# Optimization experiments

Measured on AMD Instinct MI355X. Metric: run time of the kernel, lower is better.

Reference implementation:

```python
import jax, jax.numpy as jnp
import numpy as np

V_DIM = 2048
Q_DIM = 1024
B = 64
K = 36


def setup_inputs() -> dict:
    key = jax.random.key(0)
    ks = jax.random.split(key, 6)
    s1 = 1.0 / np.sqrt(2 * V_DIM + Q_DIM)
    s2 = 1.0 / np.sqrt(V_DIM)
    s3 = 1.0 / np.sqrt(Q_DIM)
    return {
        "v": jax.random.normal(ks[0], (B, K, V_DIM), dtype=jnp.float32),
        "q": jax.random.normal(ks[1], (B, Q_DIM), dtype=jnp.float32),
        "W1": jax.random.normal(ks[2], (V_DIM, 2 * V_DIM + Q_DIM), dtype=jnp.float32) * s1,
        "b1": jnp.zeros((V_DIM,), dtype=jnp.float32),
        "W2": jax.random.normal(ks[3], (V_DIM, V_DIM), dtype=jnp.float32) * s2,
        "b2": jnp.zeros((V_DIM,), dtype=jnp.float32),
        "W3": jax.random.normal(ks[4], (Q_DIM, Q_DIM), dtype=jnp.float32) * s3,
        "b3": jnp.zeros((Q_DIM,), dtype=jnp.float32),
    }


def reference(v, q, W1, b1, W2, b2, W3, b3):
    # FCNet = (weight-normed) Linear + ReLU; dropout disabled (eval / p=0).
    vd = W2.shape[0]
    # q embedding: [B, q_dim]
    q_emb = jax.nn.relu(q @ W3.T + b3)
    # Decompose linear1(concat(v_i, v_j, q_emb)) into three matmuls.
    Wa = W1[:, :vd]            # acts on v_i
    Wb = W1[:, vd:2 * vd]      # acts on v_j
    Wc = W1[:, 2 * vd:]        # acts on q_emb
    a = jnp.einsum('bkd,vd->bkv', v, Wa)          # [B, K, v_dim]
    bpart = jnp.einsum('bkd,vd->bkv', v, Wb)      # [B, K, v_dim]
    c = jnp.einsum('bq,vq->bv', q_emb, Wc) + b1   # [B, v_dim]
    # Pairwise ReLU then sum over j: [B, K_i, K_j, v_dim] -> [B, K, v_dim]
    pair = jax.nn.relu(a[:, :, None, :] + bpart[:, None, :, :] + c[:, None, None, :])
    x = jnp.sum(pair, axis=2)
    # linear2 + ReLU
    return jax.nn.relu(jnp.einsum('bkv,wv->bkw', x, W2) + b2)
```

## Files before the change

### kernel.cpp

```cpp
#include <hip/hip_runtime.h>

#define V_DIMC 2048
#define Q_DIMC 1024
#define BATCH  64
#define KC     36
#define MROWS  (BATCH * KC)
#define W1LD   (2 * V_DIMC + Q_DIMC)

typedef __bf16 bf16_t;
typedef __attribute__((ext_vector_type(8))) __bf16 bf16x8;
typedef __attribute__((ext_vector_type(4))) __bf16 bf16x4;
typedef __attribute__((ext_vector_type(4))) float f32x4;

__device__ __forceinline__ void gload16(const bf16_t* g, bf16_t* l) {
    __builtin_amdgcn_global_load_lds(
        (const __attribute__((address_space(1))) unsigned int*)(g),
        (__attribute__((address_space(3))) unsigned int*)(l), 16, 0, 0);
}

#define MFMAI(a, b, c) __builtin_amdgcn_mfma_f32_16x16x32_bf16(a, b, c, 0, 0, 0)
#define BARX() __builtin_amdgcn_s_barrier()
#define LGKM0() asm volatile("s_waitcnt lgkmcnt(0)" ::: "memory")
#define VMC(n)  asm volatile("s_waitcnt vmcnt(" #n ")" ::: "memory")

__global__ __launch_bounds__(256) void conv_all(const float* __restrict__ v,
                                                const float* __restrict__ q,
                                                const float* __restrict__ W1,
                                                const float* __restrict__ W2,
                                                const float* __restrict__ W3,
                                                bf16_t* __restrict__ Wab,
                                                bf16_t* __restrict__ W2b,
                                                bf16_t* __restrict__ vb,
                                                bf16_t* __restrict__ W3b,
                                                bf16_t* __restrict__ Wcb,
                                                bf16_t* __restrict__ qb) {
    const int t = blockIdx.x * 256 + threadIdx.x;
    const float* src;
    bf16_t* dst;
    if (t < 2097152) {
        size_t idx = (size_t)t * 4;
        int row = (int)(idx >> 11), col = (int)(idx & 2047);
        src = (row < 2048) ? W1 + (size_t)row * W1LD + col
                           : W1 + (size_t)(row - 2048) * W1LD + V_DIMC + col;
        dst = Wab + idx;
    } else if (t < 3145728) {
        size_t idx = (size_t)(t - 2097152) * 4;
        src = W2 + idx; dst = W2b + idx;
    } else if (t < 4325376) {
        size_t idx = (size_t)(t - 3145728) * 4;
        src = v + idx; dst = vb + idx;
    } else if (t < 4587520) {
        size_t idx = (size_t)(t - 4325376) * 4;
        src = W3 + idx; dst = W3b + idx;
    } else if (t < 5111808) {
        size_t idx = (size_t)(t - 4587520) * 4;
        int row = (int)(idx >> 10), col = (int)(idx & 1023);
        src = W1 + (size_t)row * W1LD + 2 * V_DIMC + col;
        dst = Wcb + idx;
    } else {
        size_t idx = (size_t)(t - 5111808) * 4;
        src = q + idx; dst = qb + idx;
    }
    float4 f = *reinterpret_cast<const float4*>(src);
    bf16x4 o;
    o[0] = (bf16_t)f.x; o[1] = (bf16_t)f.y; o[2] = (bf16_t)f.z; o[3] = (bf16_t)f.w;
    *reinterpret_cast<bf16x4*>(dst) = o;
}

template <int NDIM, int KDIM, int MODE>
__global__ __launch_bounds__(256) void mfma_gemm64(const bf16_t* __restrict__ A,
                                                   const bf16_t* __restrict__ B,
                                                   void* __restrict__ out,
                                                   const float* __restrict__ bias) {
    __shared__ bf16_t As[64][32];
    __shared__ bf16_t Bs[128][32];
    const int n0 = blockIdx.x * 128;
    const int tid = threadIdx.x;
    const int w = tid >> 6, l = tid & 63;
    const int srow = tid >> 2;
    const int scol = (tid & 3) * 8;
    const bf16_t* Ag  = A + (size_t)srow * KDIM + scol;
    const bf16_t* Bg0 = B + (size_t)(n0 + srow) * KDIM + scol;
    const bf16_t* Bg1 = B + (size_t)(n0 + 64 + srow) * KDIM + scol;
    bf16_t* ldsA  = &As[w * 16][0];
    bf16_t* ldsB0 = &Bs[w * 16][0];
    bf16_t* ldsB1 = &Bs[64 + w * 16][0];
    const int fr = l & 15, fko = (l >> 4) * 8;

    f32x4 acc[4][2] = {};
    for (int k0 = 0; k0 < KDIM; k0 += 32) {
        gload16(Ag + k0, ldsA);
        gload16(Bg0 + k0, ldsB0);
        gload16(Bg1 + k0, ldsB1);
        __syncthreads();
        bf16x8 af[4], bfr[2];
#pragma unroll
        for (int m = 0; m < 4; ++m)
            af[m] = *reinterpret_cast<const bf16x8*>(&As[m * 16 + fr][fko]);
#pragma unroll
        for (int n = 0; n < 2; ++n)
            bfr[n] = *reinterpret_cast<const bf16x8*>(&Bs[w * 32 + n * 16 + fr][fko]);
#pragma unroll
        for (int m = 0; m < 4; ++m)
#pragma unroll
            for (int n = 0; n < 2; ++n)
                acc[m][n] = MFMAI(af[m], bfr[n], acc[m][n]);
        __syncthreads();
    }
    const int col = l & 15, rb = (l >> 4) * 4;
#pragma unroll
    for (int m = 0; m < 4; ++m)
#pragma unroll
        for (int n = 0; n < 2; ++n) {
            const int gn = n0 + w * 32 + n * 16 + col;
            const float bs = bias[gn];
#pragma unroll
            for (int r = 0; r < 4; ++r) {
                const int gm = m * 16 + rb + r;
                const float val = acc[m][n][r];
                if (MODE == 0)
                    ((bf16_t*)out)[(size_t)gm * NDIM + gn] = (bf16_t)fmaxf(val + bs, 0.f);
                else
                    ((float*)out)[(size_t)gm * NDIM + gn] = val + bs;
            }
        }
}

template <int MODE>
__global__ __launch_bounds__(512) void gemm8p(const bf16_t* __restrict__ A,
                                              const bf16_t* __restrict__ Bm,
                                              bf16_t* __restrict__ out0,
                                              bf16_t* __restrict__ out1,
                                              bf16_t* __restrict__ out2) {
    constexpr int K = 2048;
    const int z = (MODE == 2) ? (int)blockIdx.z : 0;
    const int NT = (MODE == 2) ? ((z == 2) ? 10 : 11) : 32;
    const int kb = (MODE == 2) ? z * 704 : 0;
    __shared__ bf16_t lds[2][4][8192];
    const int tid = threadIdx.x;
    const int w = tid >> 6, l = tid & 63;
    const int wm = w >> 2, wn = w & 3;
    const int m0 = blockIdx.y * 256;
    const int n0 = blockIdx.x * 256;
    const size_t sK = (size_t)K;

    const int arow = tid >> 3;
    const bf16_t* gA = A + (size_t)(m0 + arow) * sK + kb
                         + (size_t)(((tid & 7) ^ (arow & 7)) << 3);
    const int brow = tid >> 2;
    const bf16_t* gB = Bm + (size_t)(n0 + brow) * sK + kb
                          + (size_t)(((tid & 3) ^ ((tid >> 3) & 3)) << 3);
    const int stW = w * 512;

#define STGA(h, T) do {                                                        \
        const bf16_t* g_ = gA + (size_t)((h) * 128) * sK + (size_t)(T) * 64;   \
        bf16_t* d_ = &lds[(T) & 1][h][stW];                                    \
        gload16(g_, d_);                                                       \
        gload16(g_ + (size_t)64 * sK, d_ + 4096);                              \
    } while (0)
#define STGB(ks, T) do {                                                       \
        const bf16_t* g_ = gB + (size_t)(T) * 64 + (ks) * 32;                  \
        bf16_t* d_ = &lds[(T) & 1][2 + (ks)][stW];                             \
        gload16(g_, d_);                                                       \
        gload16(g_ + (size_t)128 * sK, d_ + 4096);                             \
    } while (0)

    const int fr = l & 15, lq = l >> 4;
    const int sw0 = (lq ^ (fr & 7)) << 4;
    const int sw1 = ((4 | lq) ^ (fr & 7)) << 4;
    const int bsw = (lq ^ ((fr >> 1) & 3)) << 4;
    const int aro = fr * 128;
    const int bro = (wn * 64 + fr) * 64 + bsw;

    f32x4 acc[8][4] = {};

    STGA(0, 0); STGA(1, 0); STGB(0, 0); STGB(1, 0);
    STGB(0, 1); STGB(1, 1);
    VMC(4);
    BARX();

    for (int T = 0; T < NT; ++T) {
        const char* pa  = (const char*)&lds[T & 1][wm][0];
        const char* pb0 = (const char*)&lds[T & 1][2][0];
        const char* pb1 = (const char*)&lds[T & 1][3][0];
        bf16x8 aF[4], bF[4];

#pragma unroll
        for (int mi = 0; mi < 4; ++mi)
            aF[mi] = *(const bf16x8*)(pa + mi * 2048 + aro + sw0);
#pragma unroll
        for (int ni = 0; ni < 4; ++ni)
            bF[ni] = *(const bf16x8*)(pb0 + bro + ni * 1024);
        if (T + 1 < NT) { STGA(0, T + 1); STGA(1, T + 1); }
        BARX(); LGKM0();
        __builtin_amdgcn_s_setprio(1);
#pragma unroll
        for (int mi = 0; mi < 4; ++mi)
#pragma unroll
            for (int ni = 0; ni < 4; ++ni)
                acc[mi][ni] = MFMAI(aF[mi], bF[ni], acc[mi][ni]);
        __builtin_amdgcn_s_setprio(0);
        BARX();

#pragma unroll
        for (int mi = 0; mi < 4; ++mi)
            aF[mi] = *(const bf16x8*)(pa + 8192 + mi * 2048 + aro + sw0);
        BARX(); LGKM0();
        __builtin_amdgcn_s_setprio(1);
#pragma unroll
        for (int mi = 0; mi < 4; ++mi)
#pragma unroll
            for (int ni = 0; ni < 4; ++ni)
                acc[4 + mi][ni] = MFMAI(aF[mi], bF[ni], acc[4 + mi][ni]);
        __builtin_amdgcn_s_setprio(0);
        BARX();

#pragma unroll
        for (int mi = 0; mi < 4; ++mi)
            aF[mi] = *(const bf16x8*)(pa + mi * 2048 + aro + sw1);
#pragma unroll
        for (int ni = 0; ni < 4; ++ni)
            bF[ni] = *(const bf16x8*)(pb1 + bro + ni * 1024);
        if (T + 2 < NT) STGB(0, T + 2);
        BARX(); LGKM0();
        __builtin_amdgcn_s_setprio(1);
#pragma unroll
        for (int mi = 0; mi < 4; ++mi)
#pragma unroll
            for (int ni = 0; ni < 4; ++ni)
                acc[mi][ni] = MFMAI(aF[mi], bF[ni], acc[mi][ni]);
        __builtin_amdgcn_s_setprio(0);
        BARX();

#pragma unroll
        for (int mi = 0; mi < 4; ++mi)
            aF[mi] = *(const bf16x8*)(pa + 8192 + mi * 2048 + aro + sw1);
        if (T + 2 < NT) STGB(1, T + 2);
        BARX(); LGKM0();
        __builtin_amdgcn_s_setprio(1);
#pragma unroll
        for (int mi = 0; mi < 4; ++mi)
#pragma unroll
            for (int ni = 0; ni < 4; ++ni)
                acc[4 + mi][ni] = MFMAI(aF[mi], bF[ni], acc[4 + mi][ni]);
        __builtin_amdgcn_s_setprio(0);
        if (T < NT - 2) { VMC(4); } else { VMC(0); }
        BARX();
    }
#undef STGA
#undef STGB

    bf16_t* o;
    int gn0;
    if (MODE == 0) {
        if (n0 < V_DIMC) { o = out0; gn0 = n0; }
        else             { o = out1; gn0 = n0 - V_DIMC; }
    } else {
        o = (z == 0) ? out0 : (z == 1) ? out1 : out2;
        gn0 = n0;
    }
    const int rb = lq * 4;
#pragma unroll
    for (int mi = 0; mi < 8; ++mi)
#pragma unroll
        for (int ni = 0; ni < 4; ++ni) {
            const size_t gm = (size_t)(m0 + wm * 128 + mi * 16 + rb);
            const int gn = gn0 + wn * 64 + ni * 16 + fr;
#pragma unroll
            for (int r = 0; r < 4; ++r)
                o[(gm + r) * V_DIMC + gn] = (bf16_t)acc[mi][ni][r];
        }
}

__global__ __launch_bounds__(256) void reduce_out(const bf16_t* __restrict__ p0,
                                                  const bf16_t* __restrict__ p1,
                                                  const bf16_t* __restrict__ p2,
                                                  const float* __restrict__ b2,
                                                  float* __restrict__ out) {
    const size_t t = (size_t)blockIdx.x * 256 + threadIdx.x;
    const size_t idx = t * 8;
    bf16x8 a = *reinterpret_cast<const bf16x8*>(p0 + idx);
    bf16x8 b = *reinterpret_cast<const bf16x8*>(p1 + idx);
    bf16x8 c = *reinterpret_cast<const bf16x8*>(p2 + idx);
    const int col = (int)(idx & (V_DIMC - 1));
    float4 r0, r1;
    float* rr[2] = {&r0.x, &r1.x};
#pragma unroll
    for (int h = 0; h < 2; ++h)
#pragma unroll
        for (int j = 0; j < 4; ++j)
            rr[h][j] = fmaxf((float)a[h * 4 + j] + (float)b[h * 4 + j] +
                             (float)c[h * 4 + j] + b2[col + h * 4 + j], 0.f);
    *reinterpret_cast<float4*>(out + idx) = r0;
    *reinterpret_cast<float4*>(out + idx + 4) = r1;
}

__global__ __launch_bounds__(256) void pair_kernel(const bf16_t* __restrict__ A,
                                                   const bf16_t* __restrict__ Bp,
                                                   const float* __restrict__ cbuf,
                                                   bf16_t* __restrict__ X) {
    const int v = blockIdx.x * 256 + threadIdx.x;
    const int b = blockIdx.y;
    const float cc = cbuf[b * V_DIMC + v];
    const bf16_t* Ab = A + (size_t)b * KC * V_DIMC + v;
    const bf16_t* Bb = Bp + (size_t)b * KC * V_DIMC + v;
    float av[KC], bv[KC];
#pragma unroll
    for (int k = 0; k < KC; ++k) {
        av[k] = (float)Ab[(size_t)k * V_DIMC] + cc;
        bv[k] = (float)Bb[(size_t)k * V_DIMC];
    }
    bf16_t* Xb = X + (size_t)b * KC * V_DIMC + v;
#pragma unroll
    for (int k = 0; k < KC; ++k) {
        float s = 0.f;
#pragma unroll
        for (int j = 0; j < KC; ++j) s += fmaxf(av[k] + bv[j], 0.f);
        Xb[(size_t)k * V_DIMC] = (bf16_t)s;
    }
}

extern "C" void kernel_launch(void* const* d_in, const int* in_sizes, int n_in,
                              void* d_out, int out_size, void* d_ws, size_t ws_size,
                              hipStream_t stream) {
    const float* v  = (const float*)d_in[0];
    const float* q  = (const float*)d_in[1];
    const float* W1 = (const float*)d_in[2];
    const float* b1 = (const float*)d_in[3];
    const float* W2 = (const float*)d_in[4];
    const float* b2 = (const float*)d_in[5];
    const float* W3 = (const float*)d_in[6];
    const float* b3 = (const float*)d_in[7];
    float* out = (float*)d_out;

    char* wsb = (char*)d_ws;
    bf16_t* Wab_b = (bf16_t*)wsb;
    bf16_t* W2b   = (bf16_t*)(wsb + 16777216ull);
    bf16_t* vb    = (bf16_t*)(wsb + 25165824ull);
    bf16_t* Abf   = (bf16_t*)(wsb + 34603008ull);
    bf16_t* W3b   = (bf16_t*)(wsb + 34603008ull);
    bf16_t* Wcb   = (bf16_t*)(wsb + 34603008ull + 2097152);
    bf16_t* qb    = (bf16_t*)(wsb + 34603008ull + 6291456);
    bf16_t* Bbf   = (bf16_t*)(wsb + 44040192ull);
    bf16_t* qemb  = (bf16_t*)(wsb + 53477376ull);
    float*  cbuf  = (float*) (wsb + 53608448ull);
    bf16_t* Xb    = Wab_b;

    conv_all<<<dim3(20032), 256, 0, stream>>>(v, q, W1, W2, W3, Wab_b, W2b, vb, W3b, Wcb, qb);
    mfma_gemm64<Q_DIMC, Q_DIMC, 0><<<dim3(Q_DIMC / 128), 256, 0, stream>>>(qb, W3b, qemb, b3);
    mfma_gemm64<V_DIMC, Q_DIMC, 1><<<dim3(V_DIMC / 128), 256, 0, stream>>>(qemb, Wcb, cbuf, b1);

    gemm8p<0><<<dim3(4096 / 256, MROWS / 256), 512, 0, stream>>>(vb, Wab_b, Abf, Bbf, nullptr);
    pair_kernel<<<dim3(V_DIMC / 256, BATCH), 256, 0, stream>>>(Abf, Bbf, cbuf, Xb);
    gemm8p<2><<<dim3(V_DIMC / 256, MROWS / 256, 3), 512, 0, stream>>>(Xb, W2b, Abf, Bbf, vb);
    reduce_out<<<dim3((MROWS * V_DIMC / 8) / 256), 256, 0, stream>>>(Abf, Bbf, vb, b2, out);
}
```

Measured before the change: 156.9 us.

## Split-K the small q GEMMs across warps and shrink first big GEMM M-tile

Replaces the small 64-row q-embedding and c GEMMs with a kernel that splits K across 8 warps, loads fragments straight from global memory, and reduces the partial sums through LDS. Each block now covers 64 output columns, giving twice as many blocks for these latency-bound GEMMs. The large v GEMM is templated on M-fragment count and uses 192-row tiles, so the grid is 12 row tiles instead of 9 and spreads better across the CUs. The trade-offs are extra LDS reduction traffic in the q GEMMs and smaller A tiles, which lower MFMA reuse per B load.

```diff
diff --git a/kernel.cpp b/kernel.cpp
--- a/kernel.cpp
+++ b/kernel.cpp
@@ -67,80 +67,94 @@
     *reinterpret_cast<bf16x4*>(dst) = o;
 }
 
-template <int NDIM, int KDIM, int MODE>
-__global__ __launch_bounds__(256) void mfma_gemm64(const bf16_t* __restrict__ A,
-                                                   const bf16_t* __restrict__ B,
-                                                   void* __restrict__ out,
-                                                   const float* __restrict__ bias) {
-    __shared__ bf16_t As[64][32];
-    __shared__ bf16_t Bs[128][32];
-    const int n0 = blockIdx.x * 128;
+template <int MODE>
+__global__ __launch_bounds__(512) void qgemm(const bf16_t* __restrict__ A,
+                                             const bf16_t* __restrict__ B,
+                                             void* __restrict__ out,
+                                             const float* __restrict__ bias) {
+    constexpr int K = 1024;
+    constexpr int NDIM = (MODE == 0) ? Q_DIMC : V_DIMC;
+    __shared__ float red[8][4096];
     const int tid = threadIdx.x;
     const int w = tid >> 6, l = tid & 63;
-    const int srow = tid >> 2;
-    const int scol = (tid & 3) * 8;
-    const bf16_t* Ag  = A + (size_t)srow * KDIM + scol;
-    const bf16_t* Bg0 = B + (size_t)(n0 + srow) * KDIM + scol;
-    const bf16_t* Bg1 = B + (size_t)(n0 + 64 + srow) * KDIM + scol;
-    bf16_t* ldsA  = &As[w * 16][0];
-    bf16_t* ldsB0 = &Bs[w * 16][0];
-    bf16_t* ldsB1 = &Bs[64 + w * 16][0];
-    const int fr = l & 15, fko = (l >> 4) * 8;
-
-    f32x4 acc[4][2] = {};
-    for (int k0 = 0; k0 < KDIM; k0 += 32) {
-        gload16(Ag + k0, ldsA);
-        gload16(Bg0 + k0, ldsB0);
-        gload16(Bg1 + k0, ldsB1);
-        __syncthreads();
-        bf16x8 af[4], bfr[2];
-#pragma unroll
-        for (int m = 0; m < 4; ++m)
-            af[m] = *reinterpret_cast<const bf16x8*>(&As[m * 16 + fr][fko]);
-#pragma unroll
-        for (int n = 0; n < 2; ++n)
-            bfr[n] = *reinterpret_cast<const bf16x8*>(&Bs[w * 32 + n * 16 + fr][fko]);
-#pragma unroll
-        for (int m = 0; m < 4; ++m)
-#pragma unroll
-            for (int n = 0; n < 2; ++n)
-                acc[m][n] = MFMAI(af[m], bfr[n], acc[m][n]);
-        __syncthreads();
-    }
-    const int col = l & 15, rb = (l >> 4) * 4;
-#pragma unroll
-    for (int m = 0; m < 4; ++m)
-#pragma unroll
-        for (int n = 0; n < 2; ++n) {
-            const int gn = n0 + w * 32 + n * 16 + col;
-            const float bs = bias[gn];
-#pragma unroll
-            for (int r = 0; r < 4; ++r) {
-                const int gm = m * 16 + rb + r;
-                const float val = acc[m][n][r];
-                if (MODE == 0)
-                    ((bf16_t*)out)[(size_t)gm * NDIM + gn] = (bf16_t)fmaxf(val + bs, 0.f);
-                else
-                    ((float*)out)[(size_t)gm * NDIM + gn] = val + bs;
-            }
-        }
-}
-
-template <int MODE>
+    const int n0 = blockIdx.x * 64;
+    const int fr = l & 15, lq = l >> 4;
+    const bf16_t* Ab = A + (size_t)(w * 128) + lq * 8;
+    const bf16_t* Bb = B + (size_t)n0 * K + (size_t)(w * 128) + lq * 8;
+
+    f32x4 acc[4][4] = {};
+#pragma unroll
+    for (int ks = 0; ks < 4; ++ks) {
+        bf16x8 aF[4], bF[4];
+#pragma unroll
+        for (int mi = 0; mi < 4; ++mi)
+            aF[mi] = *(const bf16x8*)(Ab + (size_t)(mi * 16 + fr) * K + ks * 32);
+#pragma unroll
+        for (int ni = 0; ni < 4; ++ni)
+            bF[ni] = *(const bf16x8*)(Bb + (size_t)(ni * 16 + fr) * K + ks * 32);
+#pragma unroll
+        for (int mi = 0; mi < 4; ++mi)
+#pragma unroll
+            for (int ni = 0; ni < 4; ++ni)
+                acc[mi][ni] = MFMAI(aF[mi], bF[ni], acc[mi][ni]);
+    }
+
+    const int rb = lq * 4;
+#pragma unroll
+    for (int mi = 0; mi < 4; ++mi)
+#pragma unroll
+        for (int ni = 0; ni < 4; ++ni)
+#pragma unroll
+            for (int j = 0; j < 4; ++j)
+                red[w][(mi * 16 + rb + j) * 64 + ni * 16 + fr] = acc[mi][ni][j];
+    __syncthreads();
+
+    const int row = tid >> 3, cb = (tid & 7) * 8;
+    float s[8] = {};
+#pragma unroll
+    for (int ww = 0; ww < 8; ++ww) {
+        f32x4 v0 = *(const f32x4*)&red[ww][row * 64 + cb];
+        f32x4 v1 = *(const f32x4*)&red[ww][row * 64 + cb + 4];
+#pragma unroll
+        for (int j = 0; j < 4; ++j) { s[j] += v0[j]; s[4 + j] += v1[j]; }
+    }
+    if (MODE == 0) {
+        bf16x8 o;
+#pragma unroll
+        for (int j = 0; j < 8; ++j)
+            o[j] = (bf16_t)fmaxf(s[j] + bias[n0 + cb + j], 0.f);
+        *reinterpret_cast<bf16x8*>((bf16_t*)out + (size_t)row * NDIM + n0 + cb) = o;
+    } else {
+        float4 r0, r1;
+        float* rr[2] = {&r0.x, &r1.x};
+#pragma unroll
+        for (int h = 0; h < 2; ++h)
+#pragma unroll
+            for (int j = 0; j < 4; ++j)
+                rr[h][j] = s[h * 4 + j] + bias[n0 + cb + h * 4 + j];
+        float* op = (float*)out + (size_t)row * NDIM + n0 + cb;
+        *reinterpret_cast<float4*>(op) = r0;
+        *reinterpret_cast<float4*>(op + 4) = r1;
+    }
+}
+
+template <int MODE, int MF>
 __global__ __launch_bounds__(512) void gemm8p(const bf16_t* __restrict__ A,
                                               const bf16_t* __restrict__ Bm,
                                               bf16_t* __restrict__ out0,
                                               bf16_t* __restrict__ out1,
                                               bf16_t* __restrict__ out2) {
     constexpr int K = 2048;
+    constexpr int MH = MF / 2;
     const int z = (MODE == 2) ? (int)blockIdx.z : 0;
     const int NT = (MODE == 2) ? ((z == 2) ? 10 : 11) : 32;
     const int kb = (MODE == 2) ? z * 704 : 0;
-    __shared__ bf16_t lds[2][4][8192];
+    __shared__ bf16_t ldsA[2][MF * 2048];
+    __shared__ bf16_t ldsB[2][2][8192];
     const int tid = threadIdx.x;
     const int w = tid >> 6, l = tid & 63;
     const int wm = w >> 2, wn = w & 3;
-    const int m0 = blockIdx.y * 256;
+    const int m0 = blockIdx.y * (MF * 32);
     const int n0 = blockIdx.x * 256;
     const size_t sK = (size_t)K;
 
@@ -152,18 +166,17 @@
                           + (size_t)(((tid & 3) ^ ((tid >> 3) & 3)) << 3);
     const int stW = w * 512;
 
-#define STGA(h, T) do {                                                        \
-        const bf16_t* g_ = gA + (size_t)((h) * 128) * sK + (size_t)(T) * 64;   \
-        bf16_t* d_ = &lds[(T) & 1][h][stW];                                    \
-        gload16(g_, d_);                                                       \
-        gload16(g_ + (size_t)64 * sK, d_ + 4096);                              \
-    } while (0)
-#define STGB(ks, T) do {                                                       \
-        const bf16_t* g_ = gB + (size_t)(T) * 64 + (ks) * 32;                  \
-        bf16_t* d_ = &lds[(T) & 1][2 + (ks)][stW];                             \
-        gload16(g_, d_);                                                       \
-        gload16(g_ + (size_t)128 * sK, d_ + 4096);                             \
-    } while (0)
+    auto STGA = [&](int T) {
+#pragma unroll
+        for (int p = 0; p < MH; ++p)
+            gload16(gA + (size_t)(p * 64) * sK + (size_t)T * 64,
+                    &ldsA[T & 1][p * 4096 + stW]);
+    };
+    auto STGB = [&](int ks, int T) {
+        const bf16_t* g_ = gB + (size_t)T * 64 + ks * 32;
+        gload16(g_, &ldsB[T & 1][ks][stW]);
+        gload16(g_ + (size_t)128 * sK, &ldsB[T & 1][ks][4096 + stW]);
+    };
 
     const int fr = l & 15, lq = l >> 4;
     const int sw0 = (lq ^ (fr & 7)) << 4;
@@ -172,30 +185,31 @@
     const int aro = fr * 128;
     const int bro = (wn * 64 + fr) * 64 + bsw;
 
-    f32x4 acc[8][4] = {};
-
-    STGA(0, 0); STGA(1, 0); STGB(0, 0); STGB(1, 0);
+    f32x4 acc[MF][4] = {};
+
+    STGA(0);
+    STGB(0, 0); STGB(1, 0);
     STGB(0, 1); STGB(1, 1);
     VMC(4);
     BARX();
 
     for (int T = 0; T < NT; ++T) {
-        const char* pa  = (const char*)&lds[T & 1][wm][0];
-        const char* pb0 = (const char*)&lds[T & 1][2][0];
-        const char* pb1 = (const char*)&lds[T & 1][3][0];
-        bf16x8 aF[4], bF[4];
-
-#pragma unroll
-        for (int mi = 0; mi < 4; ++mi)
+        const char* pa  = (const char*)&ldsA[T & 1][0] + wm * (MF * 2048);
+        const char* pb0 = (const char*)&ldsB[T & 1][0][0];
+        const char* pb1 = (const char*)&ldsB[T & 1][1][0];
+        bf16x8 aF[MH], bF[4];
+
+#pragma unroll
+        for (int mi = 0; mi < MH; ++mi)
             aF[mi] = *(const bf16x8*)(pa + mi * 2048 + aro + sw0);
 #pragma unroll
         for (int ni = 0; ni < 4; ++ni)
             bF[ni] = *(const bf16x8*)(pb0 + bro + ni * 1024);
-        if (T + 1 < NT) { STGA(0, T + 1); STGA(1, T + 1); }
+        if (T + 1 < NT) STGA(T + 1);
         BARX(); LGKM0();
         __builtin_amdgcn_s_setprio(1);
 #pragma unroll
-        for (int mi = 0; mi < 4; ++mi)
+        for (int mi = 0; mi < MH; ++mi)
 #pragma unroll
             for (int ni = 0; ni < 4; ++ni)
                 acc[mi][ni] = MFMAI(aF[mi], bF[ni], acc[mi][ni]);
@@ -203,20 +217,20 @@
         BARX();
 
 #pragma unroll
-        for (int mi = 0; mi < 4; ++mi)
-            aF[mi] = *(const bf16x8*)(pa + 8192 + mi * 2048 + aro + sw0);
+        for (int mi = 0; mi < MH; ++mi)
+            aF[mi] = *(const bf16x8*)(pa + MF * 1024 + mi * 2048 + aro + sw0);
         BARX(); LGKM0();
         __builtin_amdgcn_s_setprio(1);
 #pragma unroll
-        for (int mi = 0; mi < 4; ++mi)
-#pragma unroll
-            for (int ni = 0; ni < 4; ++ni)
-                acc[4 + mi][ni] = MFMAI(aF[mi], bF[ni], acc[4 + mi][ni]);
+        for (int mi = 0; mi < MH; ++mi)
+#pragma unroll
+            for (int ni = 0; ni < 4; ++ni)
+                acc[MH + mi][ni] = MFMAI(aF[mi], bF[ni], acc[MH + mi][ni]);
         __builtin_amdgcn_s_setprio(0);
         BARX();
 
 #pragma unroll
-        for (int mi = 0; mi < 4; ++mi)
+        for (int mi = 0; mi < MH; ++mi)
             aF[mi] = *(const bf16x8*)(pa + mi * 2048 + aro + sw1);
 #pragma unroll
         for (int ni = 0; ni < 4; ++ni)
@@ -225,7 +239,7 @@
         BARX(); LGKM0();
         __builtin_amdgcn_s_setprio(1);
 #pragma unroll
-        for (int mi = 0; mi < 4; ++mi)
+        for (int mi = 0; mi < MH; ++mi)
 #pragma unroll
             for (int ni = 0; ni < 4; ++ni)
                 acc[mi][ni] = MFMAI(aF[mi], bF[ni], acc[mi][ni]);
@@ -233,22 +247,20 @@
         BARX();
 
 #pragma unroll
-        for (int mi = 0; mi < 4; ++mi)
-            aF[mi] = *(const bf16x8*)(pa + 8192 + mi * 2048 + aro + sw1);
+        for (int mi = 0; mi < MH; ++mi)
+            aF[mi] = *(const bf16x8*)(pa + MF * 1024 + mi * 2048 + aro + sw1);
         if (T + 2 < NT) STGB(1, T + 2);
         BARX(); LGKM0();
         __builtin_amdgcn_s_setprio(1);
 #pragma unroll
-        for (int mi = 0; mi < 4; ++mi)
-#pragma unroll
-            for (int ni = 0; ni < 4; ++ni)
-                acc[4 + mi][ni] = MFMAI(aF[mi], bF[ni], acc[4 + mi][ni]);
+        for (int mi = 0; mi < MH; ++mi)
+#pragma unroll
+            for (int ni = 0; ni < 4; ++ni)
+                acc[MH + mi][ni] = MFMAI(aF[mi], bF[ni], acc[MH + mi][ni]);
         __builtin_amdgcn_s_setprio(0);
         if (T < NT - 2) { VMC(4); } else { VMC(0); }
         BARX();
     }
-#undef STGA
-#undef STGB
 
     bf16_t* o;
     int gn0;
@@ -261,10 +273,10 @@
     }
     const int rb = lq * 4;
 #pragma unroll
-    for (int mi = 0; mi < 8; ++mi)
+    for (int mi = 0; mi < MF; ++mi)
 #pragma unroll
         for (int ni = 0; ni < 4; ++ni) {
-            const size_t gm = (size_t)(m0 + wm * 128 + mi * 16 + rb);
+            const size_t gm = (size_t)(m0 + wm * (MF * 16) + mi * 16 + rb);
             const int gn = gn0 + wn * 64 + ni * 16 + fr;
 #pragma unroll
             for (int r = 0; r < 4; ++r)
@@ -347,11 +359,11 @@
     bf16_t* Xb    = Wab_b;
 
     conv_all<<<dim3(20032), 256, 0, stream>>>(v, q, W1, W2, W3, Wab_b, W2b, vb, W3b, Wcb, qb);
-    mfma_gemm64<Q_DIMC, Q_DIMC, 0><<<dim3(Q_DIMC / 128), 256, 0, stream>>>(qb, W3b, qemb, b3);
-    mfma_gemm64<V_DIMC, Q_DIMC, 1><<<dim3(V_DIMC / 128), 256, 0, stream>>>(qemb, Wcb, cbuf, b1);
-
-    gemm8p<0><<<dim3(4096 / 256, MROWS / 256), 512, 0, stream>>>(vb, Wab_b, Abf, Bbf, nullptr);
+    qgemm<0><<<dim3(Q_DIMC / 64), 512, 0, stream>>>(qb, W3b, qemb, b3);
+    qgemm<1><<<dim3(V_DIMC / 64), 512, 0, stream>>>(qemb, Wcb, cbuf, b1);
+
+    gemm8p<0, 6><<<dim3(4096 / 256, MROWS / 192), 512, 0, stream>>>(vb, Wab_b, Abf, Bbf, nullptr);
     pair_kernel<<<dim3(V_DIMC / 256, BATCH), 256, 0, stream>>>(Abf, Bbf, cbuf, Xb);
-    gemm8p<2><<<dim3(V_DIMC / 256, MROWS / 256, 3), 512, 0, stream>>>(Xb, W2b, Abf, Bbf, vb);
+    gemm8p<2, 8><<<dim3(V_DIMC / 256, MROWS / 256, 3), 512, 0, stream>>>(Xb, W2b, Abf, Bbf, vb);
     reduce_out<<<dim3((MROWS * V_DIMC / 8) / 256), 256, 0, stream>>>(Abf, Bbf, vb, b2, out);
 }
```

New measurement: 147.1 us. 1.07x faster.
